# Optimization experiments

Hardware: AMD Instinct MI355X
Metric: run time of the kernel (lower is better)

## Reference

```python
import jax, jax.numpy as jnp
import numpy as np

EMBED_DIM = 1024
NUM_HEADS = 16
DIM_K = EMBED_DIM // NUM_HEADS
B, S = 2, 2048


def setup_inputs() -> dict:
    key = jax.random.key(0)
    ks = jax.random.split(key, 7)
    scale = 1.0 / np.sqrt(EMBED_DIM)
    return {
        "query": jax.random.normal(ks[0], (B, S, EMBED_DIM), dtype=jnp.float32),
        "key": jax.random.normal(ks[1], (B, S, EMBED_DIM), dtype=jnp.float32),
        "value": jax.random.normal(ks[2], (B, S, EMBED_DIM), dtype=jnp.float32),
        "Wq": jax.random.normal(ks[3], (EMBED_DIM, EMBED_DIM), dtype=jnp.float32) * scale,
        "Wk": jax.random.normal(ks[4], (EMBED_DIM, EMBED_DIM), dtype=jnp.float32) * scale,
        "Wv": jax.random.normal(ks[5], (EMBED_DIM, EMBED_DIM), dtype=jnp.float32) * scale,
        "Wo": jax.random.normal(ks[6], (EMBED_DIM, EMBED_DIM), dtype=jnp.float32) * scale,
    }


def reference(query, key, value, Wq, Wk, Wv, Wo):
    b, s, e = query.shape
    # nn.Linear: y = x @ W.T  (bias=False)
    def proj(x, W):
        y = x @ W.T  # [b, s, e]
        return y.reshape(b, -1, NUM_HEADS, DIM_K).transpose(0, 2, 1, 3)  # [b, h, s, dk]

    q = proj(query, Wq)
    k = proj(key, Wk)
    v = proj(value, Wv)

    # attention: scores = q k^T / sqrt(dk); softmax; @ v  (dropout p=0 in eval)
    scores = jnp.einsum("bhqd,bhkd->bhqk", q, k) / jnp.sqrt(jnp.float32(DIM_K))
    attn = jax.nn.softmax(scores, axis=-1)
    x = jnp.einsum("bhqk,bhkd->bhqd", attn, v)  # [b, h, s, dk]

    x = x.transpose(0, 2, 1, 3).reshape(b, -1, e)  # merge heads
    return x @ Wo.T
```

## Files before the change

### kernel.cpp

```cpp
#include <hip/hip_runtime.h>
#include <hip/hip_bf16.h>
#include <stdint.h>

#define EMBED 1024
#define NHEAD 16
#define DKD   64
#define BATCH 2
#define SEQ   2048
#define MROWS (BATCH*SEQ)

typedef __attribute__((ext_vector_type(8))) short bf16x8;
typedef __attribute__((ext_vector_type(4))) float f32x4;
typedef unsigned short u16;
typedef unsigned int   u32;

__device__ inline u16 f2bf(float f) {
  return __builtin_bit_cast(u16, __float2bfloat16(f));
}

__device__ inline void gload_lds16(const u16* g, u16* l) {
  __builtin_amdgcn_global_load_lds(
      (const __attribute__((address_space(1))) u32*)(const void*)g,
      (__attribute__((address_space(3))) u32*)(void*)l, 16, 0, 0);
}

__global__ __launch_bounds__(256) void cast_all(
    const float* __restrict__ s0, const float* __restrict__ s1,
    const float* __restrict__ s2, const float* __restrict__ s3,
    const float* __restrict__ s4, const float* __restrict__ s5,
    const float* __restrict__ s6,
    u16* __restrict__ d0, u16* __restrict__ d1, u16* __restrict__ d2,
    u16* __restrict__ d3, u16* __restrict__ d4, u16* __restrict__ d5,
    u16* __restrict__ d6) {
  const int y = blockIdx.y;
  const float* s; u16* d; int n4;
  switch (y) {
    case 0: s = s0; d = d0; n4 = MROWS*EMBED/4; break;
    case 1: s = s1; d = d1; n4 = MROWS*EMBED/4; break;
    case 2: s = s2; d = d2; n4 = MROWS*EMBED/4; break;
    case 3: s = s3; d = d3; n4 = EMBED*EMBED/4; break;
    case 4: s = s4; d = d4; n4 = EMBED*EMBED/4; break;
    case 5: s = s5; d = d5; n4 = EMBED*EMBED/4; break;
    default: s = s6; d = d6; n4 = EMBED*EMBED/4; break;
  }
  int i = blockIdx.x * 256 + threadIdx.x;
  int stride = gridDim.x * 256;
  for (int idx = i; idx < n4; idx += stride) {
    float4 f = ((const float4*)s)[idx];
    ushort4 o;
    o.x = f2bf(f.x); o.y = f2bf(f.y); o.z = f2bf(f.z); o.w = f2bf(f.w);
    ((ushort4*)d)[idx] = o;
  }
}

__global__ __launch_bounds__(256)
void gemm_qkv(const u16* __restrict__ A0, const u16* __restrict__ A1,
              const u16* __restrict__ A2, const u16* __restrict__ B0,
              const u16* __restrict__ B1, const u16* __restrict__ B2,
              u16* __restrict__ C0, u16* __restrict__ C1, u16* __restrict__ C2) {
  constexpr int K = EMBED;
  __shared__ u16 As[128 * 32];
  __shared__ u16 Bs[128 * 32];
  const int z = blockIdx.z;
  const u16* A = (z == 0) ? A0 : (z == 1) ? A1 : A2;
  const u16* B = (z == 0) ? B0 : (z == 1) ? B1 : B2;
  u16* C       = (z == 0) ? C0 : (z == 1) ? C1 : C2;

  const int t = threadIdx.x;
  const int w = t >> 6, l = t & 63;
  const int lr = l & 15, lg = l >> 4;
  const int m0 = blockIdx.x * 128;
  const int n0 = blockIdx.y * 128;
  const int wr = (w >> 1) * 64, wc = (w & 1) * 64;

  f32x4 acc[4][4] = {};

  const int srow = t >> 2;
  const int scol = (t & 3) * 8;
  const u16* Ag = A + (size_t)(m0 + srow) * K + scol;
  const u16* Bg = B + (size_t)(n0 + srow) * K + scol;
  u16* AsW = As + w * 512;
  u16* BsW = Bs + w * 512;
  const size_t rowstep = (size_t)64 * K;

  for (int k0 = 0; k0 < K; k0 += 32) {
    gload_lds16(Ag + k0,           AsW);
    gload_lds16(Ag + k0 + rowstep, AsW + 64 * 32);
    gload_lds16(Bg + k0,           BsW);
    gload_lds16(Bg + k0 + rowstep, BsW + 64 * 32);
    __syncthreads();
    bf16x8 a[4], b[4];
#pragma unroll
    for (int r = 0; r < 4; r++)
      a[r] = *(const bf16x8*)(As + (wr + r * 16 + lr) * 32 + 8 * lg);
#pragma unroll
    for (int c = 0; c < 4; c++)
      b[c] = *(const bf16x8*)(Bs + (wc + c * 16 + lr) * 32 + 8 * lg);
#pragma unroll
    for (int r = 0; r < 4; r++)
#pragma unroll
      for (int c = 0; c < 4; c++)
        acc[r][c] = __builtin_amdgcn_mfma_f32_16x16x32_bf16(a[r], b[c], acc[r][c], 0, 0, 0);
    __syncthreads();
  }

#pragma unroll
  for (int r = 0; r < 4; r++)
#pragma unroll
    for (int c = 0; c < 4; c++)
#pragma unroll
      for (int j = 0; j < 4; j++) {
        int m = m0 + wr + r * 16 + lg * 4 + j;
        int n = n0 + wc + c * 16 + lr;
        int b_ = m >> 11, s_ = m & 2047;
        int h_ = n >> 6,  d_ = n & 63;
        u16 vv = f2bf(acc[r][c][j]);
        if (z == 2)
          C[((size_t)(b_ * NHEAD + h_) * DKD + d_) * SEQ + s_] = vv;
        else
          C[(((size_t)(b_ * NHEAD + h_) * SEQ + s_) << 6) + d_] = vv;
      }
}

__global__ __launch_bounds__(256)
void gemm_out(const u16* __restrict__ A, const u16* __restrict__ B,
              float* __restrict__ C) {
  constexpr int K = EMBED, N = EMBED;
  __shared__ u16 As[64 * 32];
  __shared__ u16 Bs[128 * 32];
  const int t = threadIdx.x;
  const int w = t >> 6, l = t & 63;
  const int lr = l & 15, lg = l >> 4;
  const int m0 = blockIdx.x * 64;
  const int n0 = blockIdx.y * 128;
  const int wr = (w >> 1) * 32, wc = (w & 1) * 64;

  f32x4 acc[2][4] = {};

  const int srow = t >> 2;
  const int scol = (t & 3) * 8;
  const u16* Ag = A + (size_t)(m0 + srow) * K + scol;
  const u16* Bg = B + (size_t)(n0 + srow) * K + scol;
  u16* AsW = As + w * 512;
  u16* BsW = Bs + w * 512;
  const size_t rowstep = (size_t)64 * K;

  for (int k0 = 0; k0 < K; k0 += 32) {
    gload_lds16(Ag + k0,           AsW);
    gload_lds16(Bg + k0,           BsW);
    gload_lds16(Bg + k0 + rowstep, BsW + 64 * 32);
    __syncthreads();
    bf16x8 a[2], b[4];
#pragma unroll
    for (int r = 0; r < 2; r++)
      a[r] = *(const bf16x8*)(As + (wr + r * 16 + lr) * 32 + 8 * lg);
#pragma unroll
    for (int c = 0; c < 4; c++)
      b[c] = *(const bf16x8*)(Bs + (wc + c * 16 + lr) * 32 + 8 * lg);
#pragma unroll
    for (int r = 0; r < 2; r++)
#pragma unroll
      for (int c = 0; c < 4; c++)
        acc[r][c] = __builtin_amdgcn_mfma_f32_16x16x32_bf16(a[r], b[c], acc[r][c], 0, 0, 0);
    __syncthreads();
  }

#pragma unroll
  for (int r = 0; r < 2; r++)
#pragma unroll
    for (int c = 0; c < 4; c++)
#pragma unroll
      for (int j = 0; j < 4; j++) {
        int m = m0 + wr + r * 16 + lg * 4 + j;
        int n = n0 + wc + c * 16 + lr;
        C[(size_t)m * N + n] = acc[r][c][j];
      }
}

__global__ __launch_bounds__(256, 2)
void attn_kernel(const u16* __restrict__ Qh, const u16* __restrict__ Kh,
                 const u16* __restrict__ Vt, u16* __restrict__ Xo) {
  __shared__ u16 KV[2][8192];
  __shared__ u16 Pl[4][32 * 64];

  const int t = threadIdx.x, w = t >> 6, l = t & 63;
  const int lr = l & 15, lg = l >> 4;
  const int xcd = blockIdx.x & 7;
  const int li  = blockIdx.x >> 3;
  const int bh  = xcd * 4 + (li >> 4);
  const int qblk = li & 15;
  const int b_ = bh >> 4, h_ = bh & 15;
  const size_t base = (size_t)bh * SEQ * DKD;
  const u16* Kb = Kh + base;
  const u16* Vb = Vt + base;
  constexpr int NT = SEQ / 64;
  constexpr float C2 = 0.18033688f;
  constexpr float THR = 44.0f;

  bf16x8 qf[2][2];
#pragma unroll
  for (int r = 0; r < 2; r++)
#pragma unroll
    for (int ks = 0; ks < 2; ks++) {
      int qrow = qblk * 128 + w * 32 + r * 16 + lr;
      qf[r][ks] = *(const bf16x8*)(Qh + base + (size_t)qrow * DKD + ks * 32 + lg * 8);
    }

  f32x4 acc[2][4] = {};
  float m2[2] = {-1e30f, -1e30f}, lsum[2] = {0.f, 0.f};
  const int sw8  = lr & 7;
  const int sw16 = sw8 << 4;

  u16* Pw = &Pl[w][0];

  auto stage = [&](int buf, int kt) {
    u16* kd = &KV[buf][0];
    u16* vd = &KV[buf][4096];
    const int rb = w * 8 + (l >> 3);
    const int sg = (l & 7) ^ (l >> 3);
#pragma unroll
    for (int ch = 0; ch < 2; ch++) {
      int row = ch * 32 + rb;
      gload_lds16(Kb + (size_t)(kt * 64 + row) * DKD + sg * 8,
                  kd + (ch * 32 + w * 8) * 64);
      gload_lds16(Vb + (size_t)row * SEQ + kt * 64 + sg * 8,
                  vd + (ch * 32 + w * 8) * 64);
    }
  };

  auto compute = [&](int buf) {
    const u16* kd = &KV[buf][0];
    const u16* vd = &KV[buf][4096];
    f32x4 s[2][4] = {};
#pragma unroll
    for (int c = 0; c < 4; c++) {
      int row = c * 16 + lr;
      bf16x8 k0 = *(const bf16x8*)(kd + row * 64 + ((lg)     ^ sw8) * 8);
      bf16x8 k1 = *(const bf16x8*)(kd + row * 64 + ((lg + 4) ^ sw8) * 8);
#pragma unroll
      for (int r = 0; r < 2; r++) {
        s[r][c] = __builtin_amdgcn_mfma_f32_16x16x32_bf16(k0, qf[r][0], s[r][c], 0, 0, 0);
        s[r][c] = __builtin_amdgcn_mfma_f32_16x16x32_bf16(k1, qf[r][1], s[r][c], 0, 0, 0);
      }
    }
    float pm[2];
#pragma unroll
    for (int r = 0; r < 2; r++) {
      float a = fmaxf(fmaxf(s[r][0][0], s[r][0][1]), fmaxf(s[r][0][2], s[r][0][3]));
      float b = fmaxf(fmaxf(s[r][1][0], s[r][1][1]), fmaxf(s[r][1][2], s[r][1][3]));
      float c = fmaxf(fmaxf(s[r][2][0], s[r][2][1]), fmaxf(s[r][2][2], s[r][2][3]));
      float d = fmaxf(fmaxf(s[r][3][0], s[r][3][1]), fmaxf(s[r][3][2], s[r][3][3]));
      pm[r] = fmaxf(fmaxf(a, b), fmaxf(c, d));
    }
    int trig = (pm[0] > m2[0] + THR) | (pm[1] > m2[1] + THR);
    if (__any(trig)) {
#pragma unroll
      for (int r = 0; r < 2; r++) {
        float pr = fmaxf(pm[r], __shfl_xor(pm[r], 16, 64));
        pr = fmaxf(pr, __shfl_xor(pr, 32, 64));
        float mn = fmaxf(m2[r], pr);
        float al = __builtin_amdgcn_exp2f((m2[r] - mn) * C2);
        lsum[r] *= al;
        m2[r] = mn;
        float alj[4];
#pragma unroll
        for (int j = 0; j < 4; j++) alj[j] = __shfl(al, 4 * lg + j, 64);
#pragma unroll
        for (int n = 0; n < 4; n++)
#pragma unroll
          for (int j = 0; j < 4; j++) acc[r][n][j] *= alj[j];
      }
    }
#pragma unroll
    for (int r = 0; r < 2; r++) {
      float nm2c = -m2[r] * C2;
      char* prow = (char*)(Pw + (r * 16 + lr) * 64);
      float ls = 0.f;
#pragma unroll
      for (int c = 0; c < 4; c++) {
        float p0 = __builtin_amdgcn_exp2f(__builtin_fmaf(s[r][c][0], C2, nm2c));
        float p1 = __builtin_amdgcn_exp2f(__builtin_fmaf(s[r][c][1], C2, nm2c));
        float p2 = __builtin_amdgcn_exp2f(__builtin_fmaf(s[r][c][2], C2, nm2c));
        float p3 = __builtin_amdgcn_exp2f(__builtin_fmaf(s[r][c][3], C2, nm2c));
        ls += (p0 + p1) + (p2 + p3);
        u32 lo = (u32)f2bf(p0) | ((u32)f2bf(p1) << 16);
        u32 hi = (u32)f2bf(p2) | ((u32)f2bf(p3) << 16);
        uint2 pk; pk.x = lo; pk.y = hi;
        *(uint2*)(prow + ((32 * c + 8 * lg) ^ sw16)) = pk;
      }
      lsum[r] += ls;
    }
    bf16x8 pf[2][2];
#pragma unroll
    for (int r = 0; r < 2; r++) {
      char* prow = (char*)(Pw + (r * 16 + lr) * 64);
#pragma unroll
      for (int ks = 0; ks < 2; ks++)
        pf[r][ks] = *(const bf16x8*)(prow + ((64 * ks + 16 * lg) ^ sw16));
    }
#pragma unroll
    for (int ks = 0; ks < 2; ks++)
#pragma unroll
      for (int n = 0; n < 4; n++) {
        bf16x8 vf = *(const bf16x8*)(vd + (n * 16 + lr) * 64 + ((lg + 4 * ks) ^ sw8) * 8);
#pragma unroll
        for (int r = 0; r < 2; r++)
          acc[r][n] = __builtin_amdgcn_mfma_f32_16x16x32_bf16(pf[r][ks], vf, acc[r][n], 0, 0, 0);
      }
  };

  stage(0, 0);
  __syncthreads();
  int cur = 0;
  for (int kt = 0; kt < NT; kt++) {
    if (kt + 1 < NT) stage(cur ^ 1, kt + 1);
    compute(cur);
    __syncthreads();
    cur ^= 1;
  }

#pragma unroll
  for (int r = 0; r < 2; r++) {
    float lv = lsum[r];
    lv += __shfl_xor(lv, 16, 64);
    lv += __shfl_xor(lv, 32, 64);
    float inv = 1.0f / lv;
    float invj[4];
#pragma unroll
    for (int j = 0; j < 4; j++) invj[j] = __shfl(inv, 4 * lg + j, 64);
#pragma unroll
    for (int n = 0; n < 4; n++)
#pragma unroll
      for (int j = 0; j < 4; j++) {
        int q = qblk * 128 + w * 32 + r * 16 + 4 * lg + j;
        Xo[((size_t)b_ * SEQ + q) * EMBED + h_ * DKD + n * 16 + lr] =
            f2bf(acc[r][n][j] * invj[j]);
      }
  }
}

extern "C" void kernel_launch(void* const* d_in, const int* in_sizes, int n_in,
                              void* d_out, int out_size, void* d_ws, size_t ws_size,
                              hipStream_t stream) {
  const float* q  = (const float*)d_in[0];
  const float* k  = (const float*)d_in[1];
  const float* v  = (const float*)d_in[2];
  const float* Wq = (const float*)d_in[3];
  const float* Wk = (const float*)d_in[4];
  const float* Wv = (const float*)d_in[5];
  const float* Wo = (const float*)d_in[6];

  char* ws = (char*)d_ws;
  const size_t SZ_X = (size_t)MROWS * EMBED * 2;
  const size_t SZ_W = (size_t)EMBED * EMBED * 2;
  u16* qbf  = (u16*)(ws);
  u16* kbf  = (u16*)(ws + SZ_X);
  u16* vbf  = (u16*)(ws + 2 * SZ_X);
  u16* wqb  = (u16*)(ws + 3 * SZ_X);
  u16* wkb  = (u16*)(ws + 3 * SZ_X + SZ_W);
  u16* wvb  = (u16*)(ws + 3 * SZ_X + 2 * SZ_W);
  u16* wob  = (u16*)(ws + 3 * SZ_X + 3 * SZ_W);
  u16* Qh   = (u16*)(ws + 3 * SZ_X + 4 * SZ_W);
  u16* Kh   = (u16*)(ws + 4 * SZ_X + 4 * SZ_W);
  u16* Vt   = (u16*)(ws + 5 * SZ_X + 4 * SZ_W);
  u16* Xcat = (u16*)(ws + 6 * SZ_X + 4 * SZ_W);

  cast_all<<<dim3(1024, 7), 256, 0, stream>>>(q, k, v, Wq, Wk, Wv, Wo,
                                              qbf, kbf, vbf, wqb, wkb, wvb, wob);

  gemm_qkv<<<dim3(MROWS / 128, EMBED / 128, 3), 256, 0, stream>>>(
      qbf, kbf, vbf, wqb, wkb, wvb, Qh, Kh, Vt);

  attn_kernel<<<512, 256, 0, stream>>>(Qh, Kh, Vt, Xcat);

  gemm_out<<<dim3(MROWS / 64, EMBED / 128), 256, 0, stream>>>(Xcat, wob, (float*)d_out);
}
```

Measured before the change: 136.8 us.

## Use 32x32x16 MFMA in attention, keep P in registers via permlane swap

```diff
diff --git a/kernel.cpp b/kernel.cpp
--- a/kernel.cpp
+++ b/kernel.cpp
@@ -9,13 +9,25 @@
 #define SEQ   2048
 #define MROWS (BATCH*SEQ)
 
-typedef __attribute__((ext_vector_type(8))) short bf16x8;
-typedef __attribute__((ext_vector_type(4))) float f32x4;
+typedef __attribute__((ext_vector_type(8)))  short bf16x8;
+typedef __attribute__((ext_vector_type(4)))  float f32x4;
+typedef __attribute__((ext_vector_type(16))) float f32x16;
 typedef unsigned short u16;
 typedef unsigned int   u32;
+typedef __attribute__((ext_vector_type(4))) u32 u32x4;
 
 __device__ inline u16 f2bf(float f) {
   return __builtin_bit_cast(u16, __float2bfloat16(f));
+}
+
+__device__ inline u32 cvtpk(float lo, float hi) {
+  u32 r;
+  asm("v_cvt_pk_bf16_f32 %0, %1, %2" : "=v"(r) : "v"(lo), "v"(hi));
+  return r;
+}
+
+__device__ inline void plswap(u32& x, u32& y) {
+  asm volatile("v_permlane32_swap_b32 %0, %1" : "+v"(x), "+v"(y));
 }
 
 __device__ inline void gload_lds16(const u16* g, u16* l) {
@@ -181,10 +193,8 @@
 void attn_kernel(const u16* __restrict__ Qh, const u16* __restrict__ Kh,
                  const u16* __restrict__ Vt, u16* __restrict__ Xo) {
   __shared__ u16 KV[2][8192];
-  __shared__ u16 Pl[4][32 * 64];
-
   const int t = threadIdx.x, w = t >> 6, l = t & 63;
-  const int lr = l & 15, lg = l >> 4;
+  const int q32 = l & 31, h = l >> 5;
   const int xcd = blockIdx.x & 7;
   const int li  = blockIdx.x >> 3;
   const int bh  = xcd * 4 + (li >> 4);
@@ -197,21 +207,14 @@
   constexpr float C2 = 0.18033688f;
   constexpr float THR = 44.0f;
 
-  bf16x8 qf[2][2];
-#pragma unroll
-  for (int r = 0; r < 2; r++)
-#pragma unroll
-    for (int ks = 0; ks < 2; ks++) {
-      int qrow = qblk * 128 + w * 32 + r * 16 + lr;
-      qf[r][ks] = *(const bf16x8*)(Qh + base + (size_t)qrow * DKD + ks * 32 + lg * 8);
-    }
-
-  f32x4 acc[2][4] = {};
-  float m2[2] = {-1e30f, -1e30f}, lsum[2] = {0.f, 0.f};
-  const int sw8  = lr & 7;
-  const int sw16 = sw8 << 4;
-
-  u16* Pw = &Pl[w][0];
+  const int qrow = qblk * 128 + w * 32 + q32;
+  bf16x8 qf[4];
+#pragma unroll
+  for (int ks = 0; ks < 4; ks++)
+    qf[ks] = *(const bf16x8*)(Qh + base + (size_t)qrow * DKD + ks * 16 + h * 8);
+
+  f32x16 acc[2] = {};
+  float m2 = -1e30f, lsum = 0.f;
 
   auto stage = [&](int buf, int kt) {
     u16* kd = &KV[buf][0];
@@ -231,82 +234,65 @@
   auto compute = [&](int buf) {
     const u16* kd = &KV[buf][0];
     const u16* vd = &KV[buf][4096];
-    f32x4 s[2][4] = {};
-#pragma unroll
-    for (int c = 0; c < 4; c++) {
-      int row = c * 16 + lr;
-      bf16x8 k0 = *(const bf16x8*)(kd + row * 64 + ((lg)     ^ sw8) * 8);
-      bf16x8 k1 = *(const bf16x8*)(kd + row * 64 + ((lg + 4) ^ sw8) * 8);
-#pragma unroll
-      for (int r = 0; r < 2; r++) {
-        s[r][c] = __builtin_amdgcn_mfma_f32_16x16x32_bf16(k0, qf[r][0], s[r][c], 0, 0, 0);
-        s[r][c] = __builtin_amdgcn_mfma_f32_16x16x32_bf16(k1, qf[r][1], s[r][c], 0, 0, 0);
+    f32x16 s[2] = {};
+#pragma unroll
+    for (int c = 0; c < 2; c++) {
+      int row = c * 32 + q32;
+#pragma unroll
+      for (int ks = 0; ks < 4; ks++) {
+        bf16x8 kf = *(const bf16x8*)(kd + row * 64 + (((2 * ks + h) ^ (row & 7)) * 8));
+        s[c] = __builtin_amdgcn_mfma_f32_32x32x16_bf16(kf, qf[ks], s[c], 0, 0, 0);
       }
     }
-    float pm[2];
-#pragma unroll
-    for (int r = 0; r < 2; r++) {
-      float a = fmaxf(fmaxf(s[r][0][0], s[r][0][1]), fmaxf(s[r][0][2], s[r][0][3]));
-      float b = fmaxf(fmaxf(s[r][1][0], s[r][1][1]), fmaxf(s[r][1][2], s[r][1][3]));
-      float c = fmaxf(fmaxf(s[r][2][0], s[r][2][1]), fmaxf(s[r][2][2], s[r][2][3]));
-      float d = fmaxf(fmaxf(s[r][3][0], s[r][3][1]), fmaxf(s[r][3][2], s[r][3][3]));
-      pm[r] = fmaxf(fmaxf(a, b), fmaxf(c, d));
-    }
-    int trig = (pm[0] > m2[0] + THR) | (pm[1] > m2[1] + THR);
-    if (__any(trig)) {
-#pragma unroll
-      for (int r = 0; r < 2; r++) {
-        float pr = fmaxf(pm[r], __shfl_xor(pm[r], 16, 64));
-        pr = fmaxf(pr, __shfl_xor(pr, 32, 64));
-        float mn = fmaxf(m2[r], pr);
-        float al = __builtin_amdgcn_exp2f((m2[r] - mn) * C2);
-        lsum[r] *= al;
-        m2[r] = mn;
-        float alj[4];
-#pragma unroll
-        for (int j = 0; j < 4; j++) alj[j] = __shfl(al, 4 * lg + j, 64);
-#pragma unroll
-        for (int n = 0; n < 4; n++)
-#pragma unroll
-          for (int j = 0; j < 4; j++) acc[r][n][j] *= alj[j];
+    bf16x8 vf[2][4];
+#pragma unroll
+    for (int dc = 0; dc < 2; dc++) {
+      int row = dc * 32 + q32;
+#pragma unroll
+      for (int tile = 0; tile < 4; tile++)
+        vf[dc][tile] = *(const bf16x8*)(vd + row * 64 + (((2 * tile + h) ^ (row & 7)) * 8));
+    }
+    float pm = s[0][0];
+#pragma unroll
+    for (int r = 1; r < 16; r++) pm = fmaxf(pm, s[0][r]);
+#pragma unroll
+    for (int r = 0; r < 16; r++) pm = fmaxf(pm, s[1][r]);
+    if (__any(pm > m2 + THR)) {
+      float pmo = __shfl_xor(pm, 32, 64);
+      float mn = fmaxf(m2, fmaxf(pm, pmo));
+      float al = __builtin_amdgcn_exp2f((m2 - mn) * C2);
+      lsum *= al;
+#pragma unroll
+      for (int dc = 0; dc < 2; dc++)
+#pragma unroll
+        for (int r = 0; r < 16; r++) acc[dc][r] *= al;
+      m2 = mn;
+    }
+    const float nm = -m2 * C2;
+    bf16x8 pfrag[4];
+    float ls = 0.f;
+#pragma unroll
+    for (int c = 0; c < 2; c++) {
+      float p[16];
+#pragma unroll
+      for (int r = 0; r < 16; r++) {
+        p[r] = __builtin_amdgcn_exp2f(__builtin_fmaf(s[c][r], C2, nm));
+        ls += p[r];
       }
-    }
-#pragma unroll
-    for (int r = 0; r < 2; r++) {
-      float nm2c = -m2[r] * C2;
-      char* prow = (char*)(Pw + (r * 16 + lr) * 64);
-      float ls = 0.f;
-#pragma unroll
-      for (int c = 0; c < 4; c++) {
-        float p0 = __builtin_amdgcn_exp2f(__builtin_fmaf(s[r][c][0], C2, nm2c));
-        float p1 = __builtin_amdgcn_exp2f(__builtin_fmaf(s[r][c][1], C2, nm2c));
-        float p2 = __builtin_amdgcn_exp2f(__builtin_fmaf(s[r][c][2], C2, nm2c));
-        float p3 = __builtin_amdgcn_exp2f(__builtin_fmaf(s[r][c][3], C2, nm2c));
-        ls += (p0 + p1) + (p2 + p3);
-        u32 lo = (u32)f2bf(p0) | ((u32)f2bf(p1) << 16);
-        u32 hi = (u32)f2bf(p2) | ((u32)f2bf(p3) << 16);
-        uint2 pk; pk.x = lo; pk.y = hi;
-        *(uint2*)(prow + ((32 * c + 8 * lg) ^ sw16)) = pk;
-      }
-      lsum[r] += ls;
-    }
-    bf16x8 pf[2][2];
-#pragma unroll
-    for (int r = 0; r < 2; r++) {
-      char* prow = (char*)(Pw + (r * 16 + lr) * 64);
-#pragma unroll
-      for (int ks = 0; ks < 2; ks++)
-        pf[r][ks] = *(const bf16x8*)(prow + ((64 * ks + 16 * lg) ^ sw16));
-    }
-#pragma unroll
-    for (int ks = 0; ks < 2; ks++)
-#pragma unroll
-      for (int n = 0; n < 4; n++) {
-        bf16x8 vf = *(const bf16x8*)(vd + (n * 16 + lr) * 64 + ((lg + 4 * ks) ^ sw8) * 8);
-#pragma unroll
-        for (int r = 0; r < 2; r++)
-          acc[r][n] = __builtin_amdgcn_mfma_f32_16x16x32_bf16(pf[r][ks], vf, acc[r][n], 0, 0, 0);
-      }
+      u32 Pk[8];
+#pragma unroll
+      for (int i = 0; i < 8; i++) Pk[i] = cvtpk(p[2 * i], p[2 * i + 1]);
+      plswap(Pk[0], Pk[2]); plswap(Pk[1], Pk[3]);
+      plswap(Pk[4], Pk[6]); plswap(Pk[5], Pk[7]);
+      pfrag[2 * c]     = __builtin_bit_cast(bf16x8, (u32x4){Pk[0], Pk[1], Pk[2], Pk[3]});
+      pfrag[2 * c + 1] = __builtin_bit_cast(bf16x8, (u32x4){Pk[4], Pk[5], Pk[6], Pk[7]});
+    }
+    lsum += ls;
+#pragma unroll
+    for (int tile = 0; tile < 4; tile++)
+#pragma unroll
+      for (int dc = 0; dc < 2; dc++)
+        acc[dc] = __builtin_amdgcn_mfma_f32_32x32x16_bf16(vf[dc][tile], pfrag[tile], acc[dc], 0, 0, 0);
   };
 
   stage(0, 0);
@@ -319,24 +305,19 @@
     cur ^= 1;
   }
 
-#pragma unroll
-  for (int r = 0; r < 2; r++) {
-    float lv = lsum[r];
-    lv += __shfl_xor(lv, 16, 64);
-    lv += __shfl_xor(lv, 32, 64);
-    float inv = 1.0f / lv;
-    float invj[4];
-#pragma unroll
-    for (int j = 0; j < 4; j++) invj[j] = __shfl(inv, 4 * lg + j, 64);
-#pragma unroll
-    for (int n = 0; n < 4; n++)
-#pragma unroll
-      for (int j = 0; j < 4; j++) {
-        int q = qblk * 128 + w * 32 + r * 16 + 4 * lg + j;
-        Xo[((size_t)b_ * SEQ + q) * EMBED + h_ * DKD + n * 16 + lr] =
-            f2bf(acc[r][n][j] * invj[j]);
-      }
-  }
+  lsum += __shfl_xor(lsum, 32, 64);
+  float inv = 1.0f / lsum;
+  u16* orow = Xo + ((size_t)b_ * SEQ + qrow) * EMBED + h_ * DKD;
+#pragma unroll
+  for (int dc = 0; dc < 2; dc++)
+#pragma unroll
+    for (int k4 = 0; k4 < 4; k4++) {
+      u32 w0 = cvtpk(acc[dc][4 * k4 + 0] * inv, acc[dc][4 * k4 + 1] * inv);
+      u32 w1 = cvtpk(acc[dc][4 * k4 + 2] * inv, acc[dc][4 * k4 + 3] * inv);
+      int d = dc * 32 + k4 * 8 + h * 4;
+      uint2 pk; pk.x = w0; pk.y = w1;
+      *(uint2*)(orow + d) = pk;
+    }
 }
 
 extern "C" void kernel_launch(void* const* d_in, const int* in_sizes, int n_in,
```

Result: faster. 122.4 us (-10.5%).
